# Kernel optimization log

Measured on AMD Instinct MI355X. Metric: run time of the kernel, lower is better.

The kernel has to match this reference:

```python
import jax, jax.numpy as jnp
import numpy as np

H = 256          # hidden_size
N_NODE = 50000   # item vocab
E_FULL = 500000  # full-graph edges
B = 1024         # sessions per batch
NODES_PER = 12   # session nodes per graph (contiguous, equal sections)
N = B * NODES_PER


def setup_inputs() -> dict:
    key = jax.random.key(0)
    ks = jax.random.split(key, 20)
    stdv = 1.0 / np.sqrt(H)
    u = lambda k, shape: jax.random.uniform(k, shape, jnp.float32, -stdv, stdv)
    return dict(
        x=jax.random.randint(ks[0], (N, 1), 1, N_NODE + 1, dtype=jnp.int32),  # 1-based item ids
        batch=jnp.repeat(jnp.arange(B, dtype=jnp.int32), NODES_PER),          # sorted graph ids
        edge_index=jax.random.randint(ks[1], (2, N), 0, N, dtype=jnp.int32),
        full_graph=jax.random.randint(ks[2], (2, E_FULL), 0, N_NODE, dtype=jnp.int32),
        emb=u(ks[3], (N_NODE, H)),
        ggnn_W=u(ks[4], (H, H)),
        gru_Wih=u(ks[5], (3 * H, H)),
        gru_Whh=u(ks[6], (3 * H, H)),
        gru_bih=u(ks[7], (3 * H,)),
        gru_bhh=u(ks[8], (3 * H,)),
        W1_w=u(ks[9], (H, H)), W1_b=u(ks[10], (H,)),
        W2_w=u(ks[11], (H, H)), W2_b=u(ks[12], (H,)),
        q_w=u(ks[13], (1, H)), q_b=u(ks[14], (1,)),
        W3_w=u(ks[15], (H, 2 * H)), W3_b=u(ks[16], (H,)),
    )


def _forward(x, batch, edge_index, full_graph, emb, ggnn_W, gru_Wih, gru_Whh,
             gru_bih, gru_bhh, W1_w, W1_b, W2_w, W2_b, q_w, q_b, W3_w, W3_b):
    # --- GatedGraphConv (num_layers=1) over the full item graph ---
    src, dst = full_graph[0], full_graph[1]
    m = emb @ ggnn_W                                      # [n_node, H]
    agg = jax.ops.segment_sum(m[src], dst, num_segments=N_NODE)  # sum aggregation
    # GRUCell(agg, emb)
    gi = agg @ gru_Wih.T + gru_bih                        # [n_node, 3H]
    gh = emb @ gru_Whh.T + gru_bhh
    i_r, i_z, i_n = jnp.split(gi, 3, axis=1)
    h_r, h_z, h_n = jnp.split(gh, 3, axis=1)
    r = jax.nn.sigmoid(i_r + h_r)
    z = jax.nn.sigmoid(i_z + h_z)
    n = jnp.tanh(i_n + r * h_n)
    hidden_all = (1.0 - z) * n + z * emb                  # [n_node, H]

    # gather session nodes (x is 1-based), relu
    h2 = jax.nn.relu(hidden_all[x[:, 0] - 1])             # [N, H]

    # --- Embedding2Score: segment attention readout ---
    sections = jax.ops.segment_sum(jnp.ones_like(batch), batch, num_segments=B)
    last_idx = jnp.cumsum(sections) - 1                   # last node of each session
    v_n = h2[last_idx]                                    # [B, H]
    v_n_rep = v_n[batch]                                  # [N, H]
    gate = jax.nn.sigmoid(v_n_rep @ W1_w.T + W1_b + h2 @ W2_w.T + W2_b)
    alpha = gate @ q_w.T + q_b                            # [N, 1]
    s_g = jax.ops.segment_sum(alpha * h2, batch, num_segments=B)  # [B, H]
    s_h = jnp.concatenate([v_n, s_g], axis=1) @ W3_w.T + W3_b     # [B, H]
    scores = s_h @ emb.T                                  # [B, n_node]
    return scores, h2


def reference(x, batch, edge_index, full_graph, emb, ggnn_W, gru_Wih, gru_Whh,
              gru_bih, gru_bhh, W1_w, W1_b, W2_w, W2_b, q_w, q_b, W3_w, W3_b):
    scores, h2 = _forward(x, batch, edge_index, full_graph, emb, ggnn_W,
                          gru_Wih, gru_Whh, gru_bih, gru_bhh,
                          W1_w, W1_b, W2_w, W2_b, q_w, q_b, W3_w, W3_b)
    return scores, h2, edge_index
```

## Files before the change

kernel.cpp:

```cpp
#include <hip/hip_runtime.h>
#include <hip/hip_bf16.h>
#include <stdint.h>

#define HDIM 256
#define NNODE 50000
#define EFULL 500000
#define BSESS 1024
#define NPER 12
#define NROWS 12288
#define CAP 96

typedef __attribute__((ext_vector_type(8))) short bf16x8;
typedef __attribute__((ext_vector_type(4))) float f32x4;
typedef __attribute__((ext_vector_type(4))) unsigned short u16x4;

__device__ __forceinline__ float bf2f(unsigned short v) {
  union { unsigned u; float f; } x; x.u = ((unsigned)v) << 16; return x.f;
}
__device__ __forceinline__ unsigned short f2bf(float f) {
  union { float f; unsigned u; } x; x.f = f;
  unsigned r = x.u + 0x7fff + ((x.u >> 16) & 1);
  return (unsigned short)(r >> 16);
}

#define CV_EMB   12800000
#define CV_GW    65536
#define CV_WIH   196608
#define CV_WHH   196608
#define CV_W1    65536
#define CV_W2    65536
#define CV_W3    131072
#define CV_BIAS  2304
#define CV_WSUM  (CV_EMB + CV_GW + CV_WIH + CV_WHH + CV_W1 + CV_W2 + CV_W3 + CV_BIAS)
#define CV_TOTAL (CV_WSUM + NNODE + NROWS + 2 * NROWS)
__global__ void k_conv(const float* __restrict__ emb, const float* __restrict__ gw,
                       const float* __restrict__ wih, const float* __restrict__ whh,
                       const float* __restrict__ w1, const float* __restrict__ w2,
                       const float* __restrict__ w3,
                       const float* __restrict__ bih, const float* __restrict__ bhh,
                       const float* __restrict__ w1b, const float* __restrict__ w2b,
                       const float* __restrict__ w3b,
                       unsigned short* __restrict__ embB, unsigned short* __restrict__ gwB,
                       unsigned short* __restrict__ wihB, unsigned short* __restrict__ whhB,
                       unsigned short* __restrict__ w1B, unsigned short* __restrict__ w2B,
                       unsigned short* __restrict__ w3B, unsigned short* __restrict__ biasB,
                       int* __restrict__ map, int* __restrict__ cnt,
                       const int* __restrict__ eidx, float* __restrict__ out_e) {
  long idx = (long)blockIdx.x * 256 + threadIdx.x;
  if (idx < CV_EMB) { embB[idx] = f2bf(emb[idx]); return; }
  idx -= CV_EMB;
  if (idx < CV_GW)  { gwB[idx] = f2bf(gw[idx]); return; }
  idx -= CV_GW;
  if (idx < CV_WIH) { wihB[idx] = f2bf(wih[idx]); return; }
  idx -= CV_WIH;
  if (idx < CV_WHH) { whhB[idx] = f2bf(whh[idx]); return; }
  idx -= CV_WHH;
  if (idx < CV_W1)  { w1B[idx] = f2bf(w1[idx]); return; }
  idx -= CV_W1;
  if (idx < CV_W2)  { w2B[idx] = f2bf(w2[idx]); return; }
  idx -= CV_W2;
  if (idx < CV_W3)  { w3B[idx] = f2bf(w3[idx]); return; }
  idx -= CV_W3;
  if (idx < CV_BIAS) {
    if (idx < 768)        { biasB[idx] = f2bf(bih[idx]); return; }
    if (idx < 1536)       { biasB[idx] = f2bf(bhh[idx - 768]); return; }
    if (idx < 1792)       { biasB[idx] = f2bf(w1b[idx - 1536]); return; }
    if (idx < 2048)       { biasB[idx] = f2bf(w2b[idx - 1792]); return; }
    biasB[idx] = f2bf(w3b[idx - 2048]); return;
  }
  idx -= CV_BIAS;
  if (idx < NNODE) { map[idx] = -1; return; }
  idx -= NNODE;
  if (idx < NROWS) { cnt[idx] = 0; return; }
  idx -= NROWS;
  if (idx < 2 * NROWS) out_e[idx] = (float)eidx[idx];
}

__global__ void k_set_map(const int* __restrict__ x, int* __restrict__ m) {
  int i = blockIdx.x * 256 + threadIdx.x;
  if (i < NROWS) atomicMax(&m[x[i] - 1], i);
}

__global__ void k_bin(const int* __restrict__ fg, const int* __restrict__ map,
                      int* __restrict__ cnt, int* __restrict__ lists) {
  int e = blockIdx.x * 256 + threadIdx.x;
  if (e >= EFULL) return;
  int cid = map[fg[EFULL + e]];
  if (cid < 0) return;
  int pos = atomicAdd(&cnt[cid], 1);
  if (pos < CAP) lists[cid * CAP + pos] = fg[e];
}

__global__ __launch_bounds__(256) void k_aggsum(const int* __restrict__ x,
                                                const int* __restrict__ map,
                                                const int* __restrict__ cnt,
                                                const int* __restrict__ lists,
                                                const float* __restrict__ emb,
                                                unsigned short* __restrict__ Acat) {
  int i = blockIdx.x * 4 + (threadIdx.x >> 6);
  int lane = threadIdx.x & 63;
  int node = x[i] - 1;
  int cid = map[node];
  int n = cnt[cid];
  const int* lp = lists + (size_t)cid * CAP;
  float sx = 0.f, sy = 0.f, sz = 0.f, sw = 0.f;
  int j = 0;
  for (; j + 4 <= n; j += 4) {
    int s0 = lp[j], s1 = lp[j + 1], s2 = lp[j + 2], s3 = lp[j + 3];
    float4 v0 = *(const float4*)(emb + (size_t)s0 * HDIM + lane * 4);
    float4 v1 = *(const float4*)(emb + (size_t)s1 * HDIM + lane * 4);
    float4 v2 = *(const float4*)(emb + (size_t)s2 * HDIM + lane * 4);
    float4 v3 = *(const float4*)(emb + (size_t)s3 * HDIM + lane * 4);
    sx += v0.x + v1.x + v2.x + v3.x;
    sy += v0.y + v1.y + v2.y + v3.y;
    sz += v0.z + v1.z + v2.z + v3.z;
    sw += v0.w + v1.w + v2.w + v3.w;
  }
  for (; j < n; j++) {
    int s0 = lp[j];
    float4 v0 = *(const float4*)(emb + (size_t)s0 * HDIM + lane * 4);
    sx += v0.x; sy += v0.y; sz += v0.z; sw += v0.w;
  }
  u16x4 o; o.x = f2bf(sx); o.y = f2bf(sy); o.z = f2bf(sz); o.w = f2bf(sw);
  *(u16x4*)(Acat + (size_t)i * 512 + lane * 4) = o;
  float4 v = *(const float4*)(emb + (size_t)node * HDIM + lane * 4);
  u16x4 o2; o2.x = f2bf(v.x); o2.y = f2bf(v.y); o2.z = f2bf(v.z); o2.w = f2bf(v.w);
  *(u16x4*)(Acat + (size_t)i * 512 + 256 + lane * 4) = o2;
}

__global__ void k_bbig(const unsigned short* __restrict__ Pt, const unsigned short* __restrict__ Whh,
                       const float* __restrict__ bih, const float* __restrict__ bhh,
                       unsigned short* __restrict__ Bbig2, unsigned short* __restrict__ bias2) {
  int idx = blockIdx.x * 256 + threadIdx.x;
  if (idx < 1024 * 512) {
    int jp = idx >> 9, k = idx & 511;
    int q = jp >> 6, g = (jp >> 4) & 3, t = jp & 15;
    int c = q * 16 + t;
    unsigned short v = 0;
    if (k < 256) {
      if (g < 3) v = Pt[(g * 256 + c) * 256 + k];
    } else {
      int kk = k - 256;
      if (g < 2) v = Whh[(g * 256 + c) * 256 + kk];
      else if (g == 3) v = Whh[(512 + c) * 256 + kk];
    }
    Bbig2[idx] = v;
    return;
  }
  int jp = idx - 1024 * 512;
  if (jp < 1024) {
    int q = jp >> 6, g = (jp >> 4) & 3, t = jp & 15;
    int c = q * 16 + t;
    float bv;
    if (g < 2)      bv = bih[g * 256 + c] + bhh[g * 256 + c];
    else if (g == 2) bv = bih[512 + c];
    else             bv = bhh[512 + c];
    bias2[jp] = f2bf(bv);
  }
}

template <bool OUT_BF16>
__device__ __forceinline__ void gemm128_body(
    unsigned short* As, unsigned short* Bs,
    const unsigned short* __restrict__ A, int lda,
    const unsigned short* __restrict__ Bm, int ldb,
    const unsigned short* __restrict__ bias,
    void* __restrict__ C, int ldc, int M, int N, int K, int bx, int by) {
  const int tid = threadIdx.x;
  const int wid = tid >> 6, lane = tid & 63;
  const int quad = lane >> 4, l15 = lane & 15;
  const int m0 = bx * 128, n0 = by * 128;
  const int wm = (wid & 1) * 64, wn = (wid >> 1) * 64;
  f32x4 acc[4][4] = {};
  const int lrow = tid >> 2;
  const int lcol = (tid & 3) * 8;
  const size_t ar0 = (size_t)min(m0 + lrow, M - 1) * lda + lcol;
  const size_t ar1 = (size_t)min(m0 + lrow + 64, M - 1) * lda + lcol;
  const size_t br0 = (size_t)min(n0 + lrow, N - 1) * ldb + lcol;
  const size_t br1 = (size_t)min(n0 + lrow + 64, N - 1) * ldb + lcol;
  const int ak = quad * 8;
  for (int k0 = 0; k0 < K; k0 += 32) {
    *(float4*)&As[(size_t)tid * 8]        = *(const float4*)&A[ar0 + k0];
    *(float4*)&As[2048 + (size_t)tid * 8] = *(const float4*)&A[ar1 + k0];
    *(float4*)&Bs[(size_t)tid * 8]        = *(const float4*)&Bm[br0 + k0];
    *(float4*)&Bs[2048 + (size_t)tid * 8] = *(const float4*)&Bm[br1 + k0];
    __syncthreads();
    bf16x8 af[4], bfv[4];
#pragma unroll
    for (int mi = 0; mi < 4; mi++) af[mi] = *(const bf16x8*)&As[(wm + mi * 16 + l15) * 32 + ak];
#pragma unroll
    for (int ni = 0; ni < 4; ni++) bfv[ni] = *(const bf16x8*)&Bs[(wn + ni * 16 + l15) * 32 + ak];
#pragma unroll
    for (int mi = 0; mi < 4; mi++)
#pragma unroll
      for (int ni = 0; ni < 4; ni++)
        acc[mi][ni] = __builtin_amdgcn_mfma_f32_16x16x32_bf16(af[mi], bfv[ni], acc[mi][ni], 0, 0, 0);
    __syncthreads();
  }
#pragma unroll
  for (int mi = 0; mi < 4; mi++) {
    const int gr0 = m0 + wm + mi * 16 + quad * 4;
#pragma unroll
    for (int ni = 0; ni < 4; ni++) {
      const int gc = n0 + wn + ni * 16 + l15;
      if (gc >= N) continue;
      const float bv = bias ? bf2f(bias[gc]) : 0.f;
#pragma unroll
      for (int r = 0; r < 4; r++) {
        const int gr = gr0 + r;
        if (gr < M) {
          const float v = acc[mi][ni][r] + bv;
          if (OUT_BF16) ((unsigned short*)C)[(size_t)gr * ldc + gc] = f2bf(v);
          else          ((float*)C)[(size_t)gr * ldc + gc] = v;
        }
      }
    }
  }
}

template <bool OUT_BF16>
__global__ __launch_bounds__(256) void k_gemm_nt(
    const unsigned short* __restrict__ A, int lda,
    const unsigned short* __restrict__ Bm, int ldb,
    const unsigned short* __restrict__ bias,
    void* __restrict__ C, int ldc, int M, int N, int K) {
  __shared__ __align__(16) unsigned short As[128 * 32];
  __shared__ __align__(16) unsigned short Bs[128 * 32];
  gemm128_body<OUT_BF16>(As, Bs, A, lda, Bm, ldb, bias, C, ldc, M, N, K, blockIdx.x, blockIdx.y);
}

__global__ __launch_bounds__(256) void k_t12(
    const unsigned short* __restrict__ h2b, const unsigned short* __restrict__ W2, const unsigned short* __restrict__ b2,
    unsigned short* __restrict__ t2,
    const unsigned short* __restrict__ shin, const unsigned short* __restrict__ W1, const unsigned short* __restrict__ b1,
    unsigned short* __restrict__ t1) {
  __shared__ __align__(16) unsigned short As[128 * 32];
  __shared__ __align__(16) unsigned short Bs[128 * 32];
  if (blockIdx.x < 96)
    gemm128_body<true>(As, Bs, h2b, HDIM, W2, HDIM, b2, t2, HDIM, NROWS, HDIM, HDIM, blockIdx.x, blockIdx.y);
  else
    gemm128_body<true>(As, Bs, shin, 512, W1, HDIM, b1, t1, HDIM, BSESS, HDIM, HDIM, blockIdx.x - 96, blockIdx.y);
}

__global__ __launch_bounds__(512) void k_ggru(
    const unsigned short* __restrict__ Acat,
    const unsigned short* __restrict__ Bbig2,
    const unsigned short* __restrict__ bias2,
    unsigned short* __restrict__ h2b, float* __restrict__ h2out,
    unsigned short* __restrict__ shin) {
  __shared__ __align__(16) unsigned short As[256 * 32];
  __shared__ __align__(16) unsigned short Bs[128 * 32];
  const int tid = threadIdx.x;
  const int wid = tid >> 6, lane = tid & 63;
  const int quad = lane >> 4, l15 = lane & 15;
  const int m0 = blockIdx.x * 256, n0 = blockIdx.y * 128;
  const int wm = (wid & 3) * 64, wn = (wid >> 2) * 64;
  f32x4 acc[4][4] = {};
  const int lrow = tid >> 2;
  const int lcol = (tid & 3) * 8;
  const size_t ar0 = (size_t)(m0 + lrow) * 512 + lcol;
  const size_t ar1 = (size_t)(m0 + lrow + 128) * 512 + lcol;
  const size_t br0 = (size_t)(n0 + lrow) * 512 + lcol;
  const int ak = quad * 8;
  for (int k0 = 0; k0 < 512; k0 += 32) {
    *(float4*)&As[(size_t)lrow * 32 + lcol]         = *(const float4*)&Acat[ar0 + k0];
    *(float4*)&As[(size_t)(lrow + 128) * 32 + lcol] = *(const float4*)&Acat[ar1 + k0];
    *(float4*)&Bs[(size_t)lrow * 32 + lcol]         = *(const float4*)&Bbig2[br0 + k0];
    __syncthreads();
    bf16x8 af[4], bfv[4];
#pragma unroll
    for (int mi = 0; mi < 4; mi++) af[mi] = *(const bf16x8*)&As[(wm + mi * 16 + l15) * 32 + ak];
#pragma unroll
    for (int g = 0; g < 4; g++) bfv[g] = *(const bf16x8*)&Bs[(wn + g * 16 + l15) * 32 + ak];
#pragma unroll
    for (int mi = 0; mi < 4; mi++)
#pragma unroll
      for (int g = 0; g < 4; g++)
        acc[mi][g] = __builtin_amdgcn_mfma_f32_16x16x32_bf16(af[mi], bfv[g], acc[mi][g], 0, 0, 0);
    __syncthreads();
  }
  const int ch = ((n0 + wn) >> 2) + l15;
  const float b0 = bf2f(bias2[(n0 + wn) + 0 * 16 + l15]);
  const float b1 = bf2f(bias2[(n0 + wn) + 1 * 16 + l15]);
  const float b2 = bf2f(bias2[(n0 + wn) + 2 * 16 + l15]);
  const float b3 = bf2f(bias2[(n0 + wn) + 3 * 16 + l15]);
#pragma unroll
  for (int mi = 0; mi < 4; mi++) {
    const int gr0 = m0 + wm + mi * 16 + quad * 4;
#pragma unroll
    for (int r = 0; r < 4; r++) {
      const int gr = gr0 + r;
      float rs = acc[mi][0][r] + b0;
      float zs = acc[mi][1][r] + b1;
      float inn = acc[mi][2][r] + b2;
      float hn = acc[mi][3][r] + b3;
      float rr = 1.f / (1.f + expf(-rs));
      float zz = 1.f / (1.f + expf(-zs));
      float nn = tanhf(inn + rr * hn);
      float e = bf2f(Acat[(size_t)gr * 512 + 256 + ch]);
      float h = fmaxf((1.f - zz) * nn + zz * e, 0.f);
      unsigned short hb = f2bf(h);
      h2b[(size_t)gr * HDIM + ch] = hb;
      h2out[(size_t)gr * HDIM + ch] = h;
      if (gr % NPER == NPER - 1) shin[(size_t)(gr / NPER) * 512 + ch] = hb;
    }
  }
}

__global__ __launch_bounds__(256) void k_attn(
    const unsigned short* __restrict__ t1, const unsigned short* __restrict__ t2,
    const unsigned short* __restrict__ h2b,
    const float* __restrict__ qw, const float* __restrict__ qb,
    unsigned short* __restrict__ shin) {
  __shared__ float al[NPER];
  const int b = blockIdx.x;
  const int w = threadIdx.x >> 6, lane = threadIdx.x & 63;
  u16x4 a = *(const u16x4*)(t1 + (size_t)b * HDIM + lane * 4);
  float4 q = *(const float4*)(qw + lane * 4);
  float ax = bf2f(a.x), ay = bf2f(a.y), az = bf2f(a.z), aw = bf2f(a.w);
#pragma unroll
  for (int i = 0; i < 3; i++) {
    int j = w * 3 + i;
    u16x4 c = *(const u16x4*)(t2 + ((size_t)b * NPER + j) * HDIM + lane * 4);
    float p = 0.f;
    p += q.x / (1.f + expf(-(ax + bf2f(c.x))));
    p += q.y / (1.f + expf(-(ay + bf2f(c.y))));
    p += q.z / (1.f + expf(-(az + bf2f(c.z))));
    p += q.w / (1.f + expf(-(aw + bf2f(c.w))));
#pragma unroll
    for (int off = 32; off > 0; off >>= 1) p += __shfl_down(p, off);
    if (lane == 0) al[j] = p + qb[0];
  }
  __syncthreads();
  const int c = threadIdx.x;
  float s = 0.f;
#pragma unroll
  for (int j = 0; j < NPER; j++)
    s += al[j] * bf2f(h2b[((size_t)b * NPER + j) * HDIM + c]);
  shin[(size_t)b * 512 + 256 + c] = f2bf(s);
}

template <bool OUT_BF16>
__global__ __launch_bounds__(512) void k_gemm_nt2(
    const unsigned short* __restrict__ A, int lda,
    const unsigned short* __restrict__ Bm, int ldb,
    const unsigned short* __restrict__ bias,
    void* __restrict__ C, int ldc, int M, int N, int K) {
  __shared__ __align__(16) unsigned short As[256 * 32];
  __shared__ __align__(16) unsigned short Bs[128 * 32];
  const int tid = threadIdx.x;
  const int wid = tid >> 6, lane = tid & 63;
  const int quad = lane >> 4, l15 = lane & 15;
  const int m0 = blockIdx.x * 256, n0 = blockIdx.y * 128;
  const int wm = (wid & 3) * 64, wn = (wid >> 2) * 64;
  f32x4 acc[4][4] = {};
  const int lrow = tid >> 2;
  const int lcol = (tid & 3) * 8;
  const size_t ar0 = (size_t)min(m0 + lrow, M - 1) * lda + lcol;
  const size_t ar1 = (size_t)min(m0 + lrow + 128, M - 1) * lda + lcol;
  const size_t br0 = (size_t)min(n0 + lrow, N - 1) * ldb + lcol;
  const int ak = quad * 8;
  for (int k0 = 0; k0 < K; k0 += 32) {
    *(float4*)&As[(size_t)lrow * 32 + lcol]         = *(const float4*)&A[ar0 + k0];
    *(float4*)&As[(size_t)(lrow + 128) * 32 + lcol] = *(const float4*)&A[ar1 + k0];
    *(float4*)&Bs[(size_t)lrow * 32 + lcol]         = *(const float4*)&Bm[br0 + k0];
    __syncthreads();
    bf16x8 af[4], bfv[4];
#pragma unroll
    for (int mi = 0; mi < 4; mi++) af[mi] = *(const bf16x8*)&As[(wm + mi * 16 + l15) * 32 + ak];
#pragma unroll
    for (int ni = 0; ni < 4; ni++) bfv[ni] = *(const bf16x8*)&Bs[(wn + ni * 16 + l15) * 32 + ak];
#pragma unroll
    for (int mi = 0; mi < 4; mi++)
#pragma unroll
      for (int ni = 0; ni < 4; ni++)
        acc[mi][ni] = __builtin_amdgcn_mfma_f32_16x16x32_bf16(af[mi], bfv[ni], acc[mi][ni], 0, 0, 0);
    __syncthreads();
  }
#pragma unroll
  for (int mi = 0; mi < 4; mi++) {
    const int gr0 = m0 + wm + mi * 16 + quad * 4;
#pragma unroll
    for (int ni = 0; ni < 4; ni++) {
      const int gc = n0 + wn + ni * 16 + l15;
      if (gc >= N) continue;
      const float bv = bias ? bf2f(bias[gc]) : 0.f;
#pragma unroll
      for (int r = 0; r < 4; r++) {
        const int gr = gr0 + r;
        if (gr < M) {
          const float v = acc[mi][ni][r] + bv;
          if (OUT_BF16) ((unsigned short*)C)[(size_t)gr * ldc + gc] = f2bf(v);
          else          ((float*)C)[(size_t)gr * ldc + gc] = v;
        }
      }
    }
  }
}

extern "C" void kernel_launch(void* const* d_in, const int* in_sizes, int n_in,
                              void* d_out, int out_size, void* d_ws, size_t ws_size,
                              hipStream_t stream) {
  const int* x     = (const int*)d_in[0];
  const int* batch = (const int*)d_in[1];
  const int* eidx  = (const int*)d_in[2];
  const int* fg    = (const int*)d_in[3];
  const float* emb   = (const float*)d_in[4];
  const float* ggnnW = (const float*)d_in[5];
  const float* Wih   = (const float*)d_in[6];
  const float* Whh   = (const float*)d_in[7];
  const float* bih   = (const float*)d_in[8];
  const float* bhh   = (const float*)d_in[9];
  const float* W1w   = (const float*)d_in[10];
  const float* W1b   = (const float*)d_in[11];
  const float* W2w   = (const float*)d_in[12];
  const float* W2b   = (const float*)d_in[13];
  const float* qw    = (const float*)d_in[14];
  const float* qb    = (const float*)d_in[15];
  const float* W3w   = (const float*)d_in[16];
  const float* W3b   = (const float*)d_in[17];
  (void)batch;

  char* w = (char*)d_ws;
  size_t off = 0;
  auto alloc = [&](size_t bytes) { char* p = w + off; off += (bytes + 511) & ~(size_t)511; return p; };
  int*            map   = (int*)alloc((size_t)NNODE * 4);
  int*            cnt   = (int*)alloc((size_t)NROWS * 4);
  int*            lists = (int*)alloc((size_t)NROWS * CAP * 4);
  unsigned short* Acat  = (unsigned short*)alloc((size_t)NROWS * 512 * 2);
  unsigned short* embB  = (unsigned short*)alloc((size_t)NNODE * HDIM * 2);
  unsigned short* gwB   = (unsigned short*)alloc((size_t)CV_GW * 2);
  unsigned short* WihB  = (unsigned short*)alloc((size_t)CV_WIH * 2);
  unsigned short* WhhB  = (unsigned short*)alloc((size_t)CV_WHH * 2);
  unsigned short* W1wB  = (unsigned short*)alloc((size_t)CV_W1 * 2);
  unsigned short* W2wB  = (unsigned short*)alloc((size_t)CV_W2 * 2);
  unsigned short* W3wB  = (unsigned short*)alloc((size_t)CV_W3 * 2);
  unsigned short* biasB = (unsigned short*)alloc((size_t)CV_BIAS * 2);
  unsigned short* Pt    = (unsigned short*)alloc((size_t)768 * 256 * 2);
  unsigned short* Bbig2 = (unsigned short*)alloc((size_t)1024 * 512 * 2);
  unsigned short* bias2 = (unsigned short*)alloc((size_t)1024 * 2);
  unsigned short* h2b   = (unsigned short*)alloc((size_t)NROWS * HDIM * 2);
  unsigned short* t1    = (unsigned short*)alloc((size_t)BSESS * HDIM * 2);
  unsigned short* t2    = (unsigned short*)alloc((size_t)NROWS * HDIM * 2);
  unsigned short* shin  = (unsigned short*)alloc((size_t)BSESS * 512 * 2);
  unsigned short* shb   = (unsigned short*)alloc((size_t)BSESS * HDIM * 2);
  if (off > ws_size) return;

  float* out_scores = (float*)d_out;
  float* out_h2     = out_scores + (size_t)BSESS * NNODE;
  float* out_e      = out_h2 + (size_t)NROWS * HDIM;

  dim3 blk(256);
  k_conv   <<<(CV_TOTAL + 255) / 256, blk, 0, stream>>>(emb, ggnnW, Wih, Whh, W1w, W2w, W3w,
               bih, bhh, W1b, W2b, W3b, embB, gwB, WihB, WhhB, W1wB, W2wB, W3wB, biasB,
               map, cnt, eidx, out_e);
  k_set_map<<<(NROWS + 255) / 256, blk, 0, stream>>>(x, map);
  k_bin    <<<(EFULL + 255) / 256, blk, 0, stream>>>(fg, map, cnt, lists);
  k_gemm_nt<true><<<dim3(6, 2), blk, 0, stream>>>(WihB, HDIM, gwB, HDIM, nullptr, Pt, HDIM, 768, HDIM, HDIM);
  k_bbig   <<<(1024 * 512 + 1024 + 255) / 256, blk, 0, stream>>>(Pt, WhhB, bih, bhh, Bbig2, bias2);
  k_aggsum <<<NROWS / 4, blk, 0, stream>>>(x, map, cnt, lists, emb, Acat);
  k_ggru   <<<dim3(48, 8), dim3(512), 0, stream>>>(Acat, Bbig2, bias2, h2b, out_h2, shin);
  k_t12    <<<dim3(104, 2), blk, 0, stream>>>(h2b, W2wB, biasB + 1792, t2, shin, W1wB, biasB + 1536, t1);
  k_attn   <<<BSESS, blk, 0, stream>>>(t1, t2, h2b, qw, qb, shin);
  k_gemm_nt<true><<<dim3(8, 2), blk, 0, stream>>>(shin, 512, W3wB, 512, biasB + 2048, shb, HDIM, BSESS, HDIM, 512);
  k_gemm_nt2<false><<<dim3(4, 391), dim3(512), 0, stream>>>(shb, HDIM, embB, HDIM, nullptr, out_scores, NNODE, BSESS, NNODE, HDIM);
}
```

Before: 474.2 us.

## Bin edges by raw destination, fuse Bbig build with GEMM, fold W3 into attention

Edges are now binned directly by destination node over all 50000 items, which removes the session map and the k_set_map launch. The trade is a larger cnt and lists workspace and atomics on every edge, and the per-list cap drops to 64. The Wih·ggnnW GEMM now writes straight into the permuted Bbig2 layout inside a combined prep kernel, removing the Pt intermediate and one launch. The W3 projection is folded into the attention kernel as a per-block dot product, replacing the separate small GEMM and the concatenated shin buffer.

```diff
diff --git a/kernel.cpp b/kernel.cpp
--- a/kernel.cpp
+++ b/kernel.cpp
@@ -8,7 +8,7 @@
 #define BSESS 1024
 #define NPER 12
 #define NROWS 12288
-#define CAP 96
+#define CAP 64
 
 typedef __attribute__((ext_vector_type(8))) short bf16x8;
 typedef __attribute__((ext_vector_type(4))) float f32x4;
@@ -32,7 +32,7 @@
 #define CV_W3    131072
 #define CV_BIAS  2304
 #define CV_WSUM  (CV_EMB + CV_GW + CV_WIH + CV_WHH + CV_W1 + CV_W2 + CV_W3 + CV_BIAS)
-#define CV_TOTAL (CV_WSUM + NNODE + NROWS + 2 * NROWS)
+#define CV_TOTAL (CV_WSUM + NNODE + 2 * NROWS)
 __global__ void k_conv(const float* __restrict__ emb, const float* __restrict__ gw,
                        const float* __restrict__ wih, const float* __restrict__ whh,
                        const float* __restrict__ w1, const float* __restrict__ w2,
@@ -44,7 +44,7 @@
                        unsigned short* __restrict__ wihB, unsigned short* __restrict__ whhB,
                        unsigned short* __restrict__ w1B, unsigned short* __restrict__ w2B,
                        unsigned short* __restrict__ w3B, unsigned short* __restrict__ biasB,
-                       int* __restrict__ map, int* __restrict__ cnt,
+                       int* __restrict__ cnt,
                        const int* __restrict__ eidx, float* __restrict__ out_e) {
   long idx = (long)blockIdx.x * 256 + threadIdx.x;
   if (idx < CV_EMB) { embB[idx] = f2bf(emb[idx]); return; }
@@ -69,30 +69,21 @@
     biasB[idx] = f2bf(w3b[idx - 2048]); return;
   }
   idx -= CV_BIAS;
-  if (idx < NNODE) { map[idx] = -1; return; }
+  if (idx < NNODE) { cnt[idx] = 0; return; }
   idx -= NNODE;
-  if (idx < NROWS) { cnt[idx] = 0; return; }
-  idx -= NROWS;
   if (idx < 2 * NROWS) out_e[idx] = (float)eidx[idx];
 }
 
-__global__ void k_set_map(const int* __restrict__ x, int* __restrict__ m) {
-  int i = blockIdx.x * 256 + threadIdx.x;
-  if (i < NROWS) atomicMax(&m[x[i] - 1], i);
-}
-
-__global__ void k_bin(const int* __restrict__ fg, const int* __restrict__ map,
+__global__ void k_bin(const int* __restrict__ fg,
                       int* __restrict__ cnt, int* __restrict__ lists) {
   int e = blockIdx.x * 256 + threadIdx.x;
   if (e >= EFULL) return;
-  int cid = map[fg[EFULL + e]];
-  if (cid < 0) return;
-  int pos = atomicAdd(&cnt[cid], 1);
-  if (pos < CAP) lists[cid * CAP + pos] = fg[e];
+  int dst = fg[EFULL + e];
+  int pos = atomicAdd(&cnt[dst], 1);
+  if (pos < CAP) lists[(size_t)dst * CAP + pos] = fg[e];
 }
 
 __global__ __launch_bounds__(256) void k_aggsum(const int* __restrict__ x,
-                                                const int* __restrict__ map,
                                                 const int* __restrict__ cnt,
                                                 const int* __restrict__ lists,
                                                 const float* __restrict__ emb,
@@ -100,9 +91,9 @@
   int i = blockIdx.x * 4 + (threadIdx.x >> 6);
   int lane = threadIdx.x & 63;
   int node = x[i] - 1;
-  int cid = map[node];
-  int n = cnt[cid];
-  const int* lp = lists + (size_t)cid * CAP;
+  int n = cnt[node];
+  if (n > CAP) n = CAP;
+  const int* lp = lists + (size_t)node * CAP;
   float sx = 0.f, sy = 0.f, sz = 0.f, sw = 0.f;
   int j = 0;
   for (; j + 4 <= n; j += 4) {
@@ -128,34 +119,88 @@
   *(u16x4*)(Acat + (size_t)i * 512 + 256 + lane * 4) = o2;
 }
 
-__global__ void k_bbig(const unsigned short* __restrict__ Pt, const unsigned short* __restrict__ Whh,
-                       const float* __restrict__ bih, const float* __restrict__ bhh,
-                       unsigned short* __restrict__ Bbig2, unsigned short* __restrict__ bias2) {
-  int idx = blockIdx.x * 256 + threadIdx.x;
-  if (idx < 1024 * 512) {
-    int jp = idx >> 9, k = idx & 511;
-    int q = jp >> 6, g = (jp >> 4) & 3, t = jp & 15;
-    int c = q * 16 + t;
+__global__ __launch_bounds__(256) void k_bprep(
+    const unsigned short* __restrict__ WihB, const unsigned short* __restrict__ gwB,
+    const unsigned short* __restrict__ WhhB,
+    const float* __restrict__ bih, const float* __restrict__ bhh,
+    unsigned short* __restrict__ Bbig2, unsigned short* __restrict__ bias2) {
+  if (blockIdx.x < 12) {
+    __shared__ __align__(16) unsigned short As[128 * 32];
+    __shared__ __align__(16) unsigned short Bs[128 * 32];
+    const int bx = blockIdx.x % 6, by = blockIdx.x / 6;
+    const int tid = threadIdx.x;
+    const int wid = tid >> 6, lane = tid & 63;
+    const int quad = lane >> 4, l15 = lane & 15;
+    const int m0 = bx * 128, n0 = by * 128;
+    const int wm = (wid & 1) * 64, wn = (wid >> 1) * 64;
+    f32x4 acc[4][4] = {};
+    const int lrow = tid >> 2;
+    const int lcol = (tid & 3) * 8;
+    const size_t ar0 = (size_t)(m0 + lrow) * HDIM + lcol;
+    const size_t ar1 = (size_t)(m0 + lrow + 64) * HDIM + lcol;
+    const size_t br0 = (size_t)(n0 + lrow) * HDIM + lcol;
+    const size_t br1 = (size_t)(n0 + lrow + 64) * HDIM + lcol;
+    const int ak = quad * 8;
+    for (int k0 = 0; k0 < HDIM; k0 += 32) {
+      *(float4*)&As[(size_t)tid * 8]        = *(const float4*)&WihB[ar0 + k0];
+      *(float4*)&As[2048 + (size_t)tid * 8] = *(const float4*)&WihB[ar1 + k0];
+      *(float4*)&Bs[(size_t)tid * 8]        = *(const float4*)&gwB[br0 + k0];
+      *(float4*)&Bs[2048 + (size_t)tid * 8] = *(const float4*)&gwB[br1 + k0];
+      __syncthreads();
+      bf16x8 af[4], bfv[4];
+#pragma unroll
+      for (int mi = 0; mi < 4; mi++) af[mi] = *(const bf16x8*)&As[(wm + mi * 16 + l15) * 32 + ak];
+#pragma unroll
+      for (int ni = 0; ni < 4; ni++) bfv[ni] = *(const bf16x8*)&Bs[(wn + ni * 16 + l15) * 32 + ak];
+#pragma unroll
+      for (int mi = 0; mi < 4; mi++)
+#pragma unroll
+        for (int ni = 0; ni < 4; ni++)
+          acc[mi][ni] = __builtin_amdgcn_mfma_f32_16x16x32_bf16(af[mi], bfv[ni], acc[mi][ni], 0, 0, 0);
+      __syncthreads();
+    }
+#pragma unroll
+    for (int mi = 0; mi < 4; mi++) {
+      const int gr0 = m0 + wm + mi * 16 + quad * 4;
+#pragma unroll
+      for (int ni = 0; ni < 4; ni++) {
+        const int gc = n0 + wn + ni * 16 + l15;
+#pragma unroll
+        for (int r = 0; r < 4; r++) {
+          const int gr = gr0 + r;
+          const int g = gr >> 8, c = gr & 255;
+          const int jp = ((c >> 4) << 6) + (g << 4) + (c & 15);
+          Bbig2[(size_t)jp * 512 + gc] = f2bf(acc[mi][ni][r]);
+        }
+      }
+    }
+    return;
+  }
+  int idx = (blockIdx.x - 12) * 256 + threadIdx.x;
+  if (idx < 262144) {
+    int jp = idx >> 8, kk = idx & 255;
+    int g = (jp >> 4) & 3, q = jp >> 6, t = jp & 15, c = q * 16 + t;
     unsigned short v = 0;
-    if (k < 256) {
-      if (g < 3) v = Pt[(g * 256 + c) * 256 + k];
-    } else {
-      int kk = k - 256;
-      if (g < 2) v = Whh[(g * 256 + c) * 256 + kk];
-      else if (g == 3) v = Whh[(512 + c) * 256 + kk];
-    }
-    Bbig2[idx] = v;
+    if (g < 2)       v = WhhB[(size_t)(g * 256 + c) * HDIM + kk];
+    else if (g == 3) v = WhhB[(size_t)(512 + c) * HDIM + kk];
+    Bbig2[(size_t)jp * 512 + 256 + kk] = v;
     return;
   }
-  int jp = idx - 1024 * 512;
-  if (jp < 1024) {
-    int q = jp >> 6, g = (jp >> 4) & 3, t = jp & 15;
-    int c = q * 16 + t;
+  idx -= 262144;
+  if (idx < 65536) {
+    int c = idx >> 8, k = idx & 255;
+    int jp = ((c >> 4) << 6) + 48 + (c & 15);
+    Bbig2[(size_t)jp * 512 + k] = 0;
+    return;
+  }
+  idx -= 65536;
+  if (idx < 1024) {
+    int q = idx >> 6, g = (idx >> 4) & 3, t = idx & 15, c = q * 16 + t;
     float bv;
-    if (g < 2)      bv = bih[g * 256 + c] + bhh[g * 256 + c];
+    if (g < 2)       bv = bih[g * 256 + c] + bhh[g * 256 + c];
     else if (g == 2) bv = bih[512 + c];
     else             bv = bhh[512 + c];
-    bias2[jp] = f2bf(bv);
+    bias2[idx] = f2bf(bv);
   }
 }
 
@@ -218,28 +263,17 @@
   }
 }
 
-template <bool OUT_BF16>
-__global__ __launch_bounds__(256) void k_gemm_nt(
-    const unsigned short* __restrict__ A, int lda,
-    const unsigned short* __restrict__ Bm, int ldb,
-    const unsigned short* __restrict__ bias,
-    void* __restrict__ C, int ldc, int M, int N, int K) {
-  __shared__ __align__(16) unsigned short As[128 * 32];
-  __shared__ __align__(16) unsigned short Bs[128 * 32];
-  gemm128_body<OUT_BF16>(As, Bs, A, lda, Bm, ldb, bias, C, ldc, M, N, K, blockIdx.x, blockIdx.y);
-}
-
 __global__ __launch_bounds__(256) void k_t12(
     const unsigned short* __restrict__ h2b, const unsigned short* __restrict__ W2, const unsigned short* __restrict__ b2,
     unsigned short* __restrict__ t2,
-    const unsigned short* __restrict__ shin, const unsigned short* __restrict__ W1, const unsigned short* __restrict__ b1,
+    const unsigned short* __restrict__ vnB, const unsigned short* __restrict__ W1, const unsigned short* __restrict__ b1,
     unsigned short* __restrict__ t1) {
   __shared__ __align__(16) unsigned short As[128 * 32];
   __shared__ __align__(16) unsigned short Bs[128 * 32];
   if (blockIdx.x < 96)
     gemm128_body<true>(As, Bs, h2b, HDIM, W2, HDIM, b2, t2, HDIM, NROWS, HDIM, HDIM, blockIdx.x, blockIdx.y);
   else
-    gemm128_body<true>(As, Bs, shin, 512, W1, HDIM, b1, t1, HDIM, BSESS, HDIM, HDIM, blockIdx.x - 96, blockIdx.y);
+    gemm128_body<true>(As, Bs, vnB, HDIM, W1, HDIM, b1, t1, HDIM, BSESS, HDIM, HDIM, blockIdx.x - 96, blockIdx.y);
 }
 
 __global__ __launch_bounds__(512) void k_ggru(
@@ -247,7 +281,7 @@
     const unsigned short* __restrict__ Bbig2,
     const unsigned short* __restrict__ bias2,
     unsigned short* __restrict__ h2b, float* __restrict__ h2out,
-    unsigned short* __restrict__ shin) {
+    unsigned short* __restrict__ vnB) {
   __shared__ __align__(16) unsigned short As[256 * 32];
   __shared__ __align__(16) unsigned short Bs[128 * 32];
   const int tid = threadIdx.x;
@@ -302,17 +336,19 @@
       unsigned short hb = f2bf(h);
       h2b[(size_t)gr * HDIM + ch] = hb;
       h2out[(size_t)gr * HDIM + ch] = h;
-      if (gr % NPER == NPER - 1) shin[(size_t)(gr / NPER) * 512 + ch] = hb;
+      if (gr % NPER == NPER - 1) vnB[(size_t)(gr / NPER) * HDIM + ch] = hb;
     }
   }
 }
 
-__global__ __launch_bounds__(256) void k_attn(
+__global__ __launch_bounds__(256) void k_attn2(
     const unsigned short* __restrict__ t1, const unsigned short* __restrict__ t2,
     const unsigned short* __restrict__ h2b,
     const float* __restrict__ qw, const float* __restrict__ qb,
-    unsigned short* __restrict__ shin) {
+    const unsigned short* __restrict__ W3, const unsigned short* __restrict__ b3,
+    unsigned short* __restrict__ shb) {
   __shared__ float al[NPER];
+  __shared__ float sh[512];
   const int b = blockIdx.x;
   const int w = threadIdx.x >> 6, lane = threadIdx.x & 63;
   u16x4 a = *(const u16x4*)(t1 + (size_t)b * HDIM + lane * 4);
@@ -331,13 +367,30 @@
     for (int off = 32; off > 0; off >>= 1) p += __shfl_down(p, off);
     if (lane == 0) al[j] = p + qb[0];
   }
+  const int c = threadIdx.x;
+  sh[c] = bf2f(h2b[((size_t)b * NPER + (NPER - 1)) * HDIM + c]);
   __syncthreads();
-  const int c = threadIdx.x;
   float s = 0.f;
 #pragma unroll
   for (int j = 0; j < NPER; j++)
     s += al[j] * bf2f(h2b[((size_t)b * NPER + j) * HDIM + c]);
-  shin[(size_t)b * 512 + 256 + c] = f2bf(s);
+  sh[256 + c] = s;
+  __syncthreads();
+  const unsigned short* wrow = W3 + (size_t)c * 512;
+  float acc = bf2f(b3[c]);
+#pragma unroll 8
+  for (int k = 0; k < 512; k += 8) {
+    bf16x8 wv = *(const bf16x8*)&wrow[k];
+    acc += bf2f((unsigned short)wv[0]) * sh[k + 0];
+    acc += bf2f((unsigned short)wv[1]) * sh[k + 1];
+    acc += bf2f((unsigned short)wv[2]) * sh[k + 2];
+    acc += bf2f((unsigned short)wv[3]) * sh[k + 3];
+    acc += bf2f((unsigned short)wv[4]) * sh[k + 4];
+    acc += bf2f((unsigned short)wv[5]) * sh[k + 5];
+    acc += bf2f((unsigned short)wv[6]) * sh[k + 6];
+    acc += bf2f((unsigned short)wv[7]) * sh[k + 7];
+  }
+  shb[(size_t)b * HDIM + c] = f2bf(acc);
 }
 
 template <bool OUT_BF16>
@@ -424,9 +477,8 @@
   char* w = (char*)d_ws;
   size_t off = 0;
   auto alloc = [&](size_t bytes) { char* p = w + off; off += (bytes + 511) & ~(size_t)511; return p; };
-  int*            map   = (int*)alloc((size_t)NNODE * 4);
-  int*            cnt   = (int*)alloc((size_t)NROWS * 4);
-  int*            lists = (int*)alloc((size_t)NROWS * CAP * 4);
+  int*            cnt   = (int*)alloc((size_t)NNODE * 4);
+  int*            lists = (int*)alloc((size_t)NNODE * CAP * 4);
   unsigned short* Acat  = (unsigned short*)alloc((size_t)NROWS * 512 * 2);
   unsigned short* embB  = (unsigned short*)alloc((size_t)NNODE * HDIM * 2);
   unsigned short* gwB   = (unsigned short*)alloc((size_t)CV_GW * 2);
@@ -436,13 +488,12 @@
   unsigned short* W2wB  = (unsigned short*)alloc((size_t)CV_W2 * 2);
   unsigned short* W3wB  = (unsigned short*)alloc((size_t)CV_W3 * 2);
   unsigned short* biasB = (unsigned short*)alloc((size_t)CV_BIAS * 2);
-  unsigned short* Pt    = (unsigned short*)alloc((size_t)768 * 256 * 2);
   unsigned short* Bbig2 = (unsigned short*)alloc((size_t)1024 * 512 * 2);
   unsigned short* bias2 = (unsigned short*)alloc((size_t)1024 * 2);
   unsigned short* h2b   = (unsigned short*)alloc((size_t)NROWS * HDIM * 2);
+  unsigned short* vnB   = (unsigned short*)alloc((size_t)BSESS * HDIM * 2);
   unsigned short* t1    = (unsigned short*)alloc((size_t)BSESS * HDIM * 2);
   unsigned short* t2    = (unsigned short*)alloc((size_t)NROWS * HDIM * 2);
-  unsigned short* shin  = (unsigned short*)alloc((size_t)BSESS * 512 * 2);
   unsigned short* shb   = (unsigned short*)alloc((size_t)BSESS * HDIM * 2);
   if (off > ws_size) return;
 
@@ -453,15 +504,12 @@
   dim3 blk(256);
   k_conv   <<<(CV_TOTAL + 255) / 256, blk, 0, stream>>>(emb, ggnnW, Wih, Whh, W1w, W2w, W3w,
                bih, bhh, W1b, W2b, W3b, embB, gwB, WihB, WhhB, W1wB, W2wB, W3wB, biasB,
-               map, cnt, eidx, out_e);
-  k_set_map<<<(NROWS + 255) / 256, blk, 0, stream>>>(x, map);
-  k_bin    <<<(EFULL + 255) / 256, blk, 0, stream>>>(fg, map, cnt, lists);
-  k_gemm_nt<true><<<dim3(6, 2), blk, 0, stream>>>(WihB, HDIM, gwB, HDIM, nullptr, Pt, HDIM, 768, HDIM, HDIM);
-  k_bbig   <<<(1024 * 512 + 1024 + 255) / 256, blk, 0, stream>>>(Pt, WhhB, bih, bhh, Bbig2, bias2);
-  k_aggsum <<<NROWS / 4, blk, 0, stream>>>(x, map, cnt, lists, emb, Acat);
-  k_ggru   <<<dim3(48, 8), dim3(512), 0, stream>>>(Acat, Bbig2, bias2, h2b, out_h2, shin);
-  k_t12    <<<dim3(104, 2), blk, 0, stream>>>(h2b, W2wB, biasB + 1792, t2, shin, W1wB, biasB + 1536, t1);
-  k_attn   <<<BSESS, blk, 0, stream>>>(t1, t2, h2b, qw, qb, shin);
-  k_gemm_nt<true><<<dim3(8, 2), blk, 0, stream>>>(shin, 512, W3wB, 512, biasB + 2048, shb, HDIM, BSESS, HDIM, 512);
+               cnt, eidx, out_e);
+  k_bin    <<<(EFULL + 255) / 256, blk, 0, stream>>>(fg, cnt, lists);
+  k_bprep  <<<12 + (262144 + 65536 + 1024 + 255) / 256, blk, 0, stream>>>(WihB, gwB, WhhB, bih, bhh, Bbig2, bias2);
+  k_aggsum <<<NROWS / 4, blk, 0, stream>>>(x, cnt, lists, emb, Acat);
+  k_ggru   <<<dim3(48, 8), dim3(512), 0, stream>>>(Acat, Bbig2, bias2, h2b, out_h2, vnB);
+  k_t12    <<<dim3(104, 2), blk, 0, stream>>>(h2b, W2wB, biasB + 1792, t2, vnB, W1wB, biasB + 1536, t1);
+  k_attn2  <<<BSESS, blk, 0, stream>>>(t1, t2, h2b, qw, qb, W3wB, biasB + 2048, shb);
   k_gemm_nt2<false><<<dim3(4, 391), dim3(512), 0, stream>>>(shb, HDIM, embB, HDIM, nullptr, out_scores, NNODE, BSESS, NNODE, HDIM);
 }
```

After: 502.4 us. 5.9% more time.
